# Kernel optimization log

Hardware: AMD Instinct MI355X
Metric: run time of the kernel (lower is better)

## Reference

```python
import jax, jax.numpy as jnp
import numpy as np

B, T, H, L, O = 128, 1024, 512, 2, 1
SCALE = 0.02  # keep tanh/sigmoid in sane range


def setup_inputs() -> dict:
    key = jax.random.key(0)
    ks = jax.random.split(key, 13)
    return {
        "input": jax.random.normal(ks[0], (B, 8), jnp.float32),
        "hidden": jax.random.normal(ks[1], (L, B, H), jnp.float32) * 0.5,
        "encoder_outputs": jax.random.normal(ks[2], (B, T, H), jnp.float32),
        "attn_w": jax.random.normal(ks[3], (1, (L + 1) * H), jnp.float32) * SCALE,
        "attn_b": jnp.zeros((1,), jnp.float32),
        "comb_w": jax.random.normal(ks[4], (H, H + O), jnp.float32) * SCALE,
        "comb_b": jnp.zeros((H,), jnp.float32),
        "gru_w_ih": jax.random.normal(ks[5], (L, 3 * H, H), jnp.float32) * SCALE,
        "gru_w_hh": jax.random.normal(ks[6], (L, 3 * H, H), jnp.float32) * SCALE,
        "gru_b_ih": jnp.zeros((L, 3 * H), jnp.float32),
        "gru_b_hh": jnp.zeros((L, 3 * H), jnp.float32),
        "out_w": jax.random.normal(ks[7], (O, H), jnp.float32) * SCALE,
        "out_b": jnp.zeros((O,), jnp.float32),
    }


def reference(input, hidden, encoder_outputs, attn_w, attn_b, comb_w, comb_b,
              gru_w_ih, gru_w_hh, gru_b_ih, gru_b_hh, out_w, out_b):
    # input0 = input[:, -1].unsqueeze(1) -> [B, 1]
    input0 = input[:, -1:]
    # hidden [L,B,H] -> hidden_attn [B, L*H]
    hidden_attn = jnp.transpose(hidden, (1, 0, 2)).reshape(hidden.shape[1], -1)
    # Vectorized additive-attention scores (original loops over T):
    # score[b,t] = [hidden_attn_b ; enc_bt] @ attn_w.T + attn_b
    w = attn_w[0]                      # [(L+1)*H]
    w_h, w_e = w[: L * H], w[L * H:]   # [L*H], [H]
    score = (hidden_attn @ w_h)[:, None] + jnp.einsum('bth,h->bt', encoder_outputs, w_e) + attn_b[0]
    attn_weights = jax.nn.softmax(score, axis=1)          # [B, T]
    attn_applied = jnp.einsum('bt,bth->bh', attn_weights, encoder_outputs)  # [B, H]
    # attn_combine + relu (dropout_p = 0 -> identity)
    comb_in = jnp.concatenate([input0, attn_applied], axis=1)  # [B, 1+H]
    x = jax.nn.relu(comb_in @ comb_w.T + comb_b)               # [B, H]
    # single-step multi-layer GRU (PyTorch gate order: r, z, n)
    new_hidden = []
    for l in range(L):
        gx = x @ gru_w_ih[l].T + gru_b_ih[l]             # [B, 3H]
        gh = hidden[l] @ gru_w_hh[l].T + gru_b_hh[l]     # [B, 3H]
        xr, xz, xn = jnp.split(gx, 3, axis=1)
        hr, hz, hn = jnp.split(gh, 3, axis=1)
        r = jax.nn.sigmoid(xr + hr)
        z = jax.nn.sigmoid(xz + hz)
        n = jnp.tanh(xn + r * hn)
        h_new = (1.0 - z) * n + z * hidden[l]
        new_hidden.append(h_new)
        x = h_new
    hidden_out = jnp.stack(new_hidden, axis=0)           # [L, B, H]
    output = x @ out_w.T + out_b                         # [B, O]
    return output, hidden_out, attn_weights[:, None, :]
```

## Files before the change

kernel.cpp:

```cpp
#include <hip/hip_runtime.h>
#include <math.h>

#define B 128
#define T 1024
#define H 512
#define L 2
#define G3H 1536

__global__ void score_kernel(const float* __restrict__ enc,
                             const float* __restrict__ attn_w,
                             float* __restrict__ score) {
    int tid  = threadIdx.x;
    int lane = tid & 63;
    int wave = tid >> 6;
    int gw = blockIdx.x * 4 + wave;
    const float4 we0 = *(const float4*)(attn_w + L * H + lane * 8);
    const float4 we1 = *(const float4*)(attn_w + L * H + lane * 8 + 4);
    size_t base = (size_t)gw * 4 * H + lane * 8;
#pragma unroll
    for (int i = 0; i < 4; i++) {
        const float4 e0 = *(const float4*)(enc + base + (size_t)i * H);
        const float4 e1 = *(const float4*)(enc + base + (size_t)i * H + 4);
        float d = e0.x * we0.x + e0.y * we0.y + e0.z * we0.z + e0.w * we0.w
                + e1.x * we1.x + e1.y * we1.y + e1.z * we1.z + e1.w * we1.w;
#pragma unroll
        for (int off = 32; off; off >>= 1) d += __shfl_xor(d, off);
        if (lane == 0) score[gw * 4 + i] = d;
    }
}

__global__ void softmax_kernel(const float* __restrict__ score,
                               float* __restrict__ attnw) {
    int b = blockIdx.x, tid = threadIdx.x;
    int lane = tid & 63, wave = tid >> 6;
    __shared__ float red[8];
    float4 v = *(const float4*)(score + b * T + tid * 4);
    float m = fmaxf(fmaxf(v.x, v.y), fmaxf(v.z, v.w));
#pragma unroll
    for (int off = 32; off; off >>= 1) m = fmaxf(m, __shfl_xor(m, off));
    if (lane == 0) red[wave] = m;
    __syncthreads();
    float M = fmaxf(fmaxf(red[0], red[1]), fmaxf(red[2], red[3]));
    float e0 = expf(v.x - M), e1 = expf(v.y - M);
    float e2 = expf(v.z - M), e3 = expf(v.w - M);
    float s = e0 + e1 + e2 + e3;
#pragma unroll
    for (int off = 32; off; off >>= 1) s += __shfl_xor(s, off);
    __syncthreads();
    if (lane == 0) red[4 + wave] = s;
    __syncthreads();
    float inv = 1.0f / (red[4] + red[5] + red[6] + red[7]);
    float4 o = {e0 * inv, e1 * inv, e2 * inv, e3 * inv};
    *(float4*)(attnw + b * T + tid * 4) = o;
}

__global__ void attn_partial_kernel(const float* __restrict__ enc,
                                    const float* __restrict__ attnw,
                                    float* __restrict__ part) {
    int tc = blockIdx.x, b = blockIdx.y, tid = threadIdx.x;
    __shared__ float wl[256];
    wl[tid] = attnw[b * T + tc * 256 + tid];
    __syncthreads();
    const float* ep = enc + ((size_t)b * T + tc * 256) * H + tid * 2;
    float2 acc = {0.0f, 0.0f};
#pragma unroll 4
    for (int t = 0; t < 256; t++) {
        float2 e = *(const float2*)(ep + (size_t)t * H);
        float w = wl[t];
        acc.x += w * e.x;
        acc.y += w * e.y;
    }
    *(float2*)(part + ((size_t)tc * B + b) * H + tid * 2) = acc;
}

__global__ void comb_kernel(const float* __restrict__ part,
                            const float* __restrict__ input,
                            const float* __restrict__ comb_w,
                            const float* __restrict__ comb_b,
                            float* __restrict__ x_out) {
    int q = blockIdx.x, b = blockIdx.y, tid = threadIdx.x;
    __shared__ float at[H];
    __shared__ float in0s;
    for (int j = tid; j < H; j += 256) {
        at[j] = part[(size_t)b * H + j]
              + part[(size_t)(B * H) + b * H + j]
              + part[(size_t)(2 * B * H) + b * H + j]
              + part[(size_t)(3 * B * H) + b * H + j];
    }
    if (tid == 0) in0s = input[b * 8 + 7];
    __syncthreads();
    int lane = tid & 63, wave = tid >> 6;
    float in0 = in0s;
    float areg[8];
#pragma unroll
    for (int j = 0; j < 8; j++) areg[j] = at[j * 64 + lane];
    for (int r = 0; r < 32; r++) {
        int h = q * 128 + wave * 32 + r;
        const float* wr = comb_w + (size_t)h * (H + 1);
        float d = 0.0f;
#pragma unroll
        for (int j = 0; j < 8; j++) d += areg[j] * wr[1 + j * 64 + lane];
#pragma unroll
        for (int off = 32; off; off >>= 1) d += __shfl_xor(d, off);
        if (lane == 0)
            x_out[(size_t)b * H + h] = fmaxf(0.0f, d + in0 * wr[0] + comb_b[h]);
    }
}

__global__ void gemm_kernel(const float* __restrict__ A0,
                            const float* __restrict__ A1,
                            const float* __restrict__ W0,
                            const float* __restrict__ W1,
                            float* __restrict__ C0,
                            float* __restrict__ C1) {
    int z = blockIdx.z;
    const float* A = z ? A1 : A0;
    const float* W = z ? W1 : W0;
    float* C = z ? C1 : C0;
    __shared__ float As[32][33];
    __shared__ float Ws[32][33];
    int n0 = blockIdx.x * 32, m0 = blockIdx.y * 32;
    int tid = threadIdx.x;
    int lrow = tid >> 3;
    int lcol = (tid & 7) * 4;
    int tm = (tid >> 4) * 2;
    int tn = (tid & 15) * 2;
    float a00 = 0, a01 = 0, a10 = 0, a11 = 0;
    for (int k0 = 0; k0 < H; k0 += 32) {
        float4 av = *(const float4*)(A + (size_t)(m0 + lrow) * H + k0 + lcol);
        float4 wv = *(const float4*)(W + (size_t)(n0 + lrow) * H + k0 + lcol);
        __syncthreads();
        As[lrow][lcol] = av.x; As[lrow][lcol + 1] = av.y;
        As[lrow][lcol + 2] = av.z; As[lrow][lcol + 3] = av.w;
        Ws[lrow][lcol] = wv.x; Ws[lrow][lcol + 1] = wv.y;
        Ws[lrow][lcol + 2] = wv.z; Ws[lrow][lcol + 3] = wv.w;
        __syncthreads();
#pragma unroll
        for (int k = 0; k < 32; k++) {
            float x0 = As[tm][k], x1 = As[tm + 1][k];
            float w0 = Ws[tn][k], w1 = Ws[tn + 1][k];
            a00 += x0 * w0; a01 += x0 * w1;
            a10 += x1 * w0; a11 += x1 * w1;
        }
    }
    C[(size_t)(m0 + tm) * G3H + n0 + tn]         = a00;
    C[(size_t)(m0 + tm) * G3H + n0 + tn + 1]     = a01;
    C[(size_t)(m0 + tm + 1) * G3H + n0 + tn]     = a10;
    C[(size_t)(m0 + tm + 1) * G3H + n0 + tn + 1] = a11;
}

__global__ void gates_kernel(const float* __restrict__ gx,
                             const float* __restrict__ gh,
                             const float* __restrict__ b_ih,
                             const float* __restrict__ b_hh,
                             const float* __restrict__ hprev,
                             float* __restrict__ hid_out,
                             float* __restrict__ x_out) {
    int idx = blockIdx.x * 256 + threadIdx.x;
    int b = idx >> 9, h = idx & 511;
    size_t gb = (size_t)b * G3H;
    float xr = gx[gb + h]         + b_ih[h];
    float xz = gx[gb + H + h]     + b_ih[H + h];
    float xn = gx[gb + 2 * H + h] + b_ih[2 * H + h];
    float hr = gh[gb + h]         + b_hh[h];
    float hz = gh[gb + H + h]     + b_hh[H + h];
    float hn = gh[gb + 2 * H + h] + b_hh[2 * H + h];
    float hp = hprev[(size_t)b * H + h];
    float r = 1.0f / (1.0f + expf(-(xr + hr)));
    float z = 1.0f / (1.0f + expf(-(xz + hz)));
    float n = tanhf(xn + r * hn);
    float hnew = (1.0f - z) * n + z * hp;
    hid_out[(size_t)b * H + h] = hnew;
    x_out[(size_t)b * H + h] = hnew;
}

__global__ void out_kernel(const float* __restrict__ x,
                           const float* __restrict__ out_w,
                           const float* __restrict__ out_b,
                           float* __restrict__ out) {
    int b = blockIdx.x, lane = threadIdx.x;
    const float4 w0 = *(const float4*)(out_w + lane * 8);
    const float4 w1 = *(const float4*)(out_w + lane * 8 + 4);
    const float4 x0 = *(const float4*)(x + (size_t)b * H + lane * 8);
    const float4 x1 = *(const float4*)(x + (size_t)b * H + lane * 8 + 4);
    float d = x0.x * w0.x + x0.y * w0.y + x0.z * w0.z + x0.w * w0.w
            + x1.x * w1.x + x1.y * w1.y + x1.z * w1.z + x1.w * w1.w;
#pragma unroll
    for (int off = 32; off; off >>= 1) d += __shfl_xor(d, off);
    if (lane == 0) out[b] = d + out_b[0];
}

extern "C" void kernel_launch(void* const* d_in, const int* in_sizes, int n_in,
                              void* d_out, int out_size, void* d_ws, size_t ws_size,
                              hipStream_t stream) {
    const float* input  = (const float*)d_in[0];
    const float* hidden = (const float*)d_in[1];
    const float* enc    = (const float*)d_in[2];
    const float* attn_w = (const float*)d_in[3];
    const float* comb_w = (const float*)d_in[5];
    const float* comb_b = (const float*)d_in[6];
    const float* w_ih   = (const float*)d_in[7];
    const float* w_hh   = (const float*)d_in[8];
    const float* b_ih   = (const float*)d_in[9];
    const float* b_hh   = (const float*)d_in[10];
    const float* out_w  = (const float*)d_in[11];
    const float* out_b  = (const float*)d_in[12];

    float* out = (float*)d_out;
    float* hid_out = out + B;
    float* attnw   = out + B + L * B * H;

    float* ws    = (float*)d_ws;
    float* score = ws;
    float* part  = score + B * T;
    float* x     = part + 4 * B * H;
    float* gx    = x + B * H;
    float* gh    = gx + B * G3H;

    score_kernel<<<dim3((B * T) / 16), 256, 0, stream>>>(enc, attn_w, score);
    softmax_kernel<<<dim3(B), 256, 0, stream>>>(score, attnw);
    attn_partial_kernel<<<dim3(4, B), 256, 0, stream>>>(enc, attnw, part);
    comb_kernel<<<dim3(4, B), 256, 0, stream>>>(part, input, comb_w, comb_b, x);

    for (int l = 0; l < L; l++) {
        const float* hl = hidden + (size_t)l * B * H;
        gemm_kernel<<<dim3(G3H / 32, B / 32, 2), 256, 0, stream>>>(
            x, hl,
            w_ih + (size_t)l * G3H * H, w_hh + (size_t)l * G3H * H,
            gx, gh);
        gates_kernel<<<dim3(B * H / 256), 256, 0, stream>>>(
            gx, gh, b_ih + l * G3H, b_hh + l * G3H, hl,
            hid_out + (size_t)l * B * H, x);
    }
    out_kernel<<<dim3(B), 64, 0, stream>>>(x, out_w, out_b, out);
}
```

Baseline: 514.3 us.

## Fuse score, softmax and weighted sum into one online-softmax pass; split-K GRU GEMMs

Replaces the separate score, softmax and attention-sum kernels with one flash-style kernel that stages encoder tiles in shared memory and keeps a running max and sum. Partial results across 8 T-chunks are merged in a small reduce kernel that also writes the normalized attention weights. This cuts the encoder tensor from two full reads to one. Separately, the GRU GEMMs use a 4-way split-K to launch more blocks, and the gates kernel sums the partial results, at the cost of extra workspace traffic. Using __expf instead of expf may change numerics slightly.

Measured after the change: 458.5 us. 1.12x faster.

```diff
diff --git a/kernel.cpp b/kernel.cpp
--- a/kernel.cpp
+++ b/kernel.cpp
@@ -6,94 +6,121 @@
 #define H 512
 #define L 2
 #define G3H 1536
-
-__global__ void score_kernel(const float* __restrict__ enc,
-                             const float* __restrict__ attn_w,
-                             float* __restrict__ score) {
-    int tid  = threadIdx.x;
-    int lane = tid & 63;
-    int wave = tid >> 6;
-    int gw = blockIdx.x * 4 + wave;
-    const float4 we0 = *(const float4*)(attn_w + L * H + lane * 8);
-    const float4 we1 = *(const float4*)(attn_w + L * H + lane * 8 + 4);
-    size_t base = (size_t)gw * 4 * H + lane * 8;
-#pragma unroll
-    for (int i = 0; i < 4; i++) {
-        const float4 e0 = *(const float4*)(enc + base + (size_t)i * H);
-        const float4 e1 = *(const float4*)(enc + base + (size_t)i * H + 4);
-        float d = e0.x * we0.x + e0.y * we0.y + e0.z * we0.z + e0.w * we0.w
-                + e1.x * we1.x + e1.y * we1.y + e1.z * we1.z + e1.w * we1.w;
-#pragma unroll
-        for (int off = 32; off; off >>= 1) d += __shfl_xor(d, off);
-        if (lane == 0) score[gw * 4 + i] = d;
-    }
-}
-
-__global__ void softmax_kernel(const float* __restrict__ score,
-                               float* __restrict__ attnw) {
+#define C 8
+#define TC 128
+#define TT 16
+#define KS 4
+
+__global__ __launch_bounds__(256, 4)
+void attn_fused_kernel(const float* __restrict__ enc,
+                       const float* __restrict__ attn_w,
+                       float* __restrict__ score_out,
+                       float* __restrict__ part,
+                       float* __restrict__ stats) {
+    int c = blockIdx.x, b = blockIdx.y;
+    int tid = threadIdx.x, lane = tid & 63, wave = tid >> 6;
+    __shared__ float tile[TT * H];
+    __shared__ float s_tile[TT];
+
+    float we[8];
+#pragma unroll
+    for (int j = 0; j < 8; j++) we[j] = attn_w[L * H + lane + j * 64];
+
+    float m_run = -1e30f, l_run = 0.0f;
+    float accx = 0.0f, accy = 0.0f;
+    const float* encb = enc + ((size_t)b * T + c * TC) * H;
+
+    for (int t0 = 0; t0 < TC; t0 += TT) {
+        __syncthreads();
+#pragma unroll
+        for (int k = 0; k < 8; k++) {
+            *(float4*)(tile + 4 * tid + k * 1024) =
+                *(const float4*)(encb + (size_t)t0 * H + 4 * tid + k * 1024);
+        }
+        __syncthreads();
+#pragma unroll
+        for (int r = 0; r < 4; r++) {
+            int row = wave * 4 + r;
+            const float* tr = tile + row * H;
+            float d = 0.0f;
+#pragma unroll
+            for (int j = 0; j < 8; j++) d += we[j] * tr[lane + j * 64];
+#pragma unroll
+            for (int off = 32; off; off >>= 1) d += __shfl_xor(d, off);
+            if (lane == 0) {
+                s_tile[row] = d;
+                score_out[b * T + c * TC + t0 + row] = d;
+            }
+        }
+        __syncthreads();
+        float s[TT], tmax = -1e30f;
+#pragma unroll
+        for (int i = 0; i < TT; i++) { s[i] = s_tile[i]; tmax = fmaxf(tmax, s[i]); }
+        float m_new = fmaxf(m_run, tmax);
+        float alpha = __expf(m_run - m_new);
+        accx *= alpha; accy *= alpha;
+        float wsum = 0.0f;
+#pragma unroll
+        for (int i = 0; i < TT; i++) {
+            float w = __expf(s[i] - m_new);
+            wsum += w;
+            accx += w * tile[i * H + tid];
+            accy += w * tile[i * H + tid + 256];
+        }
+        l_run = l_run * alpha + wsum;
+        m_run = m_new;
+    }
+    part[((size_t)c * B + b) * H + tid]       = accx;
+    part[((size_t)c * B + b) * H + tid + 256] = accy;
+    if (tid == 0) {
+        stats[(c * B + b) * 2]     = m_run;
+        stats[(c * B + b) * 2 + 1] = l_run;
+    }
+}
+
+__global__ void attn_reduce_kernel(const float* __restrict__ part,
+                                   const float* __restrict__ stats,
+                                   const float* __restrict__ score,
+                                   float* __restrict__ attn_applied,
+                                   float* __restrict__ attnw) {
     int b = blockIdx.x, tid = threadIdx.x;
-    int lane = tid & 63, wave = tid >> 6;
-    __shared__ float red[8];
-    float4 v = *(const float4*)(score + b * T + tid * 4);
-    float m = fmaxf(fmaxf(v.x, v.y), fmaxf(v.z, v.w));
-#pragma unroll
-    for (int off = 32; off; off >>= 1) m = fmaxf(m, __shfl_xor(m, off));
-    if (lane == 0) red[wave] = m;
-    __syncthreads();
-    float M = fmaxf(fmaxf(red[0], red[1]), fmaxf(red[2], red[3]));
-    float e0 = expf(v.x - M), e1 = expf(v.y - M);
-    float e2 = expf(v.z - M), e3 = expf(v.w - M);
-    float s = e0 + e1 + e2 + e3;
-#pragma unroll
-    for (int off = 32; off; off >>= 1) s += __shfl_xor(s, off);
-    __syncthreads();
-    if (lane == 0) red[4 + wave] = s;
-    __syncthreads();
-    float inv = 1.0f / (red[4] + red[5] + red[6] + red[7]);
-    float4 o = {e0 * inv, e1 * inv, e2 * inv, e3 * inv};
-    *(float4*)(attnw + b * T + tid * 4) = o;
-}
-
-__global__ void attn_partial_kernel(const float* __restrict__ enc,
-                                    const float* __restrict__ attnw,
-                                    float* __restrict__ part) {
-    int tc = blockIdx.x, b = blockIdx.y, tid = threadIdx.x;
-    __shared__ float wl[256];
-    wl[tid] = attnw[b * T + tc * 256 + tid];
-    __syncthreads();
-    const float* ep = enc + ((size_t)b * T + tc * 256) * H + tid * 2;
-    float2 acc = {0.0f, 0.0f};
-#pragma unroll 4
-    for (int t = 0; t < 256; t++) {
-        float2 e = *(const float2*)(ep + (size_t)t * H);
-        float w = wl[t];
-        acc.x += w * e.x;
-        acc.y += w * e.y;
-    }
-    *(float2*)(part + ((size_t)tc * B + b) * H + tid * 2) = acc;
-}
-
-__global__ void comb_kernel(const float* __restrict__ part,
+    float mc[C], lc[C], m_fin = -1e30f;
+#pragma unroll
+    for (int k = 0; k < C; k++) {
+        mc[k] = stats[(k * B + b) * 2];
+        lc[k] = stats[(k * B + b) * 2 + 1];
+        m_fin = fmaxf(m_fin, mc[k]);
+    }
+    float l_fin = 0.0f;
+#pragma unroll
+    for (int k = 0; k < C; k++) l_fin += lc[k] * __expf(mc[k] - m_fin);
+    float inv = 1.0f / l_fin;
+    float ax = 0.0f, ay = 0.0f;
+#pragma unroll
+    for (int k = 0; k < C; k++) {
+        float sc = __expf(mc[k] - m_fin);
+        ax += sc * part[((size_t)k * B + b) * H + tid];
+        ay += sc * part[((size_t)k * B + b) * H + tid + 256];
+    }
+    attn_applied[(size_t)b * H + tid]       = ax * inv;
+    attn_applied[(size_t)b * H + tid + 256] = ay * inv;
+    float4 sv = *(const float4*)(score + b * T + tid * 4);
+    float4 ov = { __expf(sv.x - m_fin) * inv, __expf(sv.y - m_fin) * inv,
+                  __expf(sv.z - m_fin) * inv, __expf(sv.w - m_fin) * inv };
+    *(float4*)(attnw + b * T + tid * 4) = ov;
+}
+
+__global__ void comb_kernel(const float* __restrict__ attn_applied,
                             const float* __restrict__ input,
                             const float* __restrict__ comb_w,
                             const float* __restrict__ comb_b,
                             float* __restrict__ x_out) {
     int q = blockIdx.x, b = blockIdx.y, tid = threadIdx.x;
-    __shared__ float at[H];
-    __shared__ float in0s;
-    for (int j = tid; j < H; j += 256) {
-        at[j] = part[(size_t)b * H + j]
-              + part[(size_t)(B * H) + b * H + j]
-              + part[(size_t)(2 * B * H) + b * H + j]
-              + part[(size_t)(3 * B * H) + b * H + j];
-    }
-    if (tid == 0) in0s = input[b * 8 + 7];
-    __syncthreads();
     int lane = tid & 63, wave = tid >> 6;
-    float in0 = in0s;
+    float in0 = input[b * 8 + 7];
     float areg[8];
 #pragma unroll
-    for (int j = 0; j < 8; j++) areg[j] = at[j * 64 + lane];
+    for (int j = 0; j < 8; j++) areg[j] = attn_applied[(size_t)b * H + j * 64 + lane];
     for (int r = 0; r < 32; r++) {
         int h = q * 128 + wave * 32 + r;
         const float* wr = comb_w + (size_t)h * (H + 1);
@@ -114,9 +141,10 @@
                             float* __restrict__ C0,
                             float* __restrict__ C1) {
     int z = blockIdx.z;
-    const float* A = z ? A1 : A0;
-    const float* W = z ? W1 : W0;
-    float* C = z ? C1 : C0;
+    int sel = z & 1, ks = z >> 1;
+    const float* A = sel ? A1 : A0;
+    const float* W = sel ? W1 : W0;
+    float* Cp = (sel ? C1 : C0) + (size_t)ks * B * G3H;
     __shared__ float As[32][33];
     __shared__ float Ws[32][33];
     int n0 = blockIdx.x * 32, m0 = blockIdx.y * 32;
@@ -126,7 +154,8 @@
     int tm = (tid >> 4) * 2;
     int tn = (tid & 15) * 2;
     float a00 = 0, a01 = 0, a10 = 0, a11 = 0;
-    for (int k0 = 0; k0 < H; k0 += 32) {
+    int kbeg = ks * (H / KS), kend = kbeg + H / KS;
+    for (int k0 = kbeg; k0 < kend; k0 += 32) {
         float4 av = *(const float4*)(A + (size_t)(m0 + lrow) * H + k0 + lcol);
         float4 wv = *(const float4*)(W + (size_t)(n0 + lrow) * H + k0 + lcol);
         __syncthreads();
@@ -143,10 +172,10 @@
             a10 += x1 * w0; a11 += x1 * w1;
         }
     }
-    C[(size_t)(m0 + tm) * G3H + n0 + tn]         = a00;
-    C[(size_t)(m0 + tm) * G3H + n0 + tn + 1]     = a01;
-    C[(size_t)(m0 + tm + 1) * G3H + n0 + tn]     = a10;
-    C[(size_t)(m0 + tm + 1) * G3H + n0 + tn + 1] = a11;
+    Cp[(size_t)(m0 + tm) * G3H + n0 + tn]         = a00;
+    Cp[(size_t)(m0 + tm) * G3H + n0 + tn + 1]     = a01;
+    Cp[(size_t)(m0 + tm + 1) * G3H + n0 + tn]     = a10;
+    Cp[(size_t)(m0 + tm + 1) * G3H + n0 + tn + 1] = a11;
 }
 
 __global__ void gates_kernel(const float* __restrict__ gx,
@@ -159,12 +188,14 @@
     int idx = blockIdx.x * 256 + threadIdx.x;
     int b = idx >> 9, h = idx & 511;
     size_t gb = (size_t)b * G3H;
-    float xr = gx[gb + h]         + b_ih[h];
-    float xz = gx[gb + H + h]     + b_ih[H + h];
-    float xn = gx[gb + 2 * H + h] + b_ih[2 * H + h];
-    float hr = gh[gb + h]         + b_hh[h];
-    float hz = gh[gb + H + h]     + b_hh[H + h];
-    float hn = gh[gb + 2 * H + h] + b_hh[2 * H + h];
+    float xr = b_ih[h], xz = b_ih[H + h], xn = b_ih[2 * H + h];
+    float hr = b_hh[h], hz = b_hh[H + h], hn = b_hh[2 * H + h];
+#pragma unroll
+    for (int k = 0; k < KS; k++) {
+        size_t o = (size_t)k * B * G3H + gb;
+        xr += gx[o + h];         xz += gx[o + H + h];     xn += gx[o + 2 * H + h];
+        hr += gh[o + h];         hz += gh[o + H + h];     hn += gh[o + 2 * H + h];
+    }
     float hp = hprev[(size_t)b * H + h];
     float r = 1.0f / (1.0f + expf(-(xr + hr)));
     float z = 1.0f / (1.0f + expf(-(xz + hz)));
@@ -210,21 +241,22 @@
     float* hid_out = out + B;
     float* attnw   = out + B + L * B * H;
 
-    float* ws    = (float*)d_ws;
-    float* score = ws;
-    float* part  = score + B * T;
-    float* x     = part + 4 * B * H;
-    float* gx    = x + B * H;
-    float* gh    = gx + B * G3H;
-
-    score_kernel<<<dim3((B * T) / 16), 256, 0, stream>>>(enc, attn_w, score);
-    softmax_kernel<<<dim3(B), 256, 0, stream>>>(score, attnw);
-    attn_partial_kernel<<<dim3(4, B), 256, 0, stream>>>(enc, attnw, part);
-    comb_kernel<<<dim3(4, B), 256, 0, stream>>>(part, input, comb_w, comb_b, x);
+    float* ws      = (float*)d_ws;
+    float* score   = ws;
+    float* part    = score + B * T;
+    float* stats   = part + C * B * H;
+    float* attnapp = stats + C * B * 2;
+    float* x       = attnapp + B * H;
+    float* gx      = x + B * H;
+    float* gh      = gx + KS * B * G3H;
+
+    attn_fused_kernel<<<dim3(C, B), 256, 0, stream>>>(enc, attn_w, score, part, stats);
+    attn_reduce_kernel<<<dim3(B), 256, 0, stream>>>(part, stats, score, attnapp, attnw);
+    comb_kernel<<<dim3(4, B), 256, 0, stream>>>(attnapp, input, comb_w, comb_b, x);
 
     for (int l = 0; l < L; l++) {
         const float* hl = hidden + (size_t)l * B * H;
-        gemm_kernel<<<dim3(G3H / 32, B / 32, 2), 256, 0, stream>>>(
+        gemm_kernel<<<dim3(G3H / 32, B / 32, 2 * KS), 256, 0, stream>>>(
             x, hl,
             w_ih + (size_t)l * G3H * H, w_hh + (size_t)l * G3H * H,
             gx, gh);
```
